# Kernel tuning notes

Measured on AMD Instinct MI355X. Metric: run time of the kernel, lower is better.

The kernel has to match this reference:

```python
import jax, jax.numpy as jnp
import numpy as np

CONF_THRES = 0.8
NMS_THRES = 0.4
IMG_SIZE = 416
MAX_DET = 3000
NEG = jnp.float32(-1e9)


def xywh2xyxy(b):
    cx, cy, w, h = b[..., 0], b[..., 1], b[..., 2], b[..., 3]
    return jnp.stack([cx - w / 2, cy - h / 2, cx + w / 2, cy + h / 2], axis=-1)


def iou_one_vs_all(box, boxes):
    # box [4], boxes [N,4]; matches original bbox_iou (+1 pixel convention, 1e-16 eps)
    ix1 = jnp.maximum(box[0], boxes[:, 0])
    iy1 = jnp.maximum(box[1], boxes[:, 1])
    ix2 = jnp.minimum(box[2], boxes[:, 2])
    iy2 = jnp.minimum(box[3], boxes[:, 3])
    inter = jnp.clip(ix2 - ix1 + 1, 0) * jnp.clip(iy2 - iy1 + 1, 0)
    a1 = (box[2] - box[0] + 1) * (box[3] - box[1] + 1)
    a2 = (boxes[:, 2] - boxes[:, 0] + 1) * (boxes[:, 3] - boxes[:, 1] + 1)
    return inter / (a1 + a2 - inter + 1e-16)


def nms_single(pred):
    # pred [N, 85] = [cx, cy, w, h, obj, 80 class scores]
    boxes = xywh2xyxy(pred[:, :4])
    obj = pred[:, 4]
    cls_conf = jnp.max(pred[:, 5:], axis=1)
    cls_id = jnp.argmax(pred[:, 5:], axis=1).astype(pred.dtype)
    valid = obj >= CONF_THRES
    score = jnp.where(valid, obj * cls_conf, NEG)
    order = jnp.argsort(-score)  # descending score, invalid pushed to end
    boxes, obj = boxes[order], obj[order]
    cls_conf, cls_id = cls_conf[order], cls_id[order]
    alive0 = valid[order]

    def step(alive, _):
        any_alive = jnp.any(alive)
        idx = jnp.argmax(alive)  # first surviving = highest remaining score
        iou = iou_one_vs_all(boxes[idx], boxes)
        invalid = (iou > NMS_THRES) & (cls_id == cls_id[idx]) & alive
        w = jnp.where(invalid, obj, 0.0)
        wsum = jnp.where(any_alive, w.sum(), 1.0)
        merged = (w[:, None] * boxes).sum(0) / wsum  # obj-weighted box merge, as original
        det = jnp.concatenate([merged, jnp.stack([obj[idx], cls_conf[idx], cls_id[idx]])])
        det = jnp.where(any_alive, det, NEG)
        return alive & ~invalid, (det, any_alive)

    _, (kept, kept_mask) = jax.lax.scan(step, alive0, None, length=MAX_DET)
    return kept, kept_mask  # kept [MAX_DET,7] = [x1,y1,x2,y2,obj,cls_conf,cls_id]


def setup_inputs() -> dict:
    key = jax.random.key(0)
    k1, k2, k3, k4 = jax.random.split(key, 4)
    B, N, C = 16, 10647, 80
    cxy = jax.random.uniform(k1, (B, N, 2), jnp.float32) * IMG_SIZE   # box centers in pixels
    wh = jax.random.uniform(k2, (B, N, 2), jnp.float32) * 80.0 + 2.0  # box sizes
    obj = jax.random.uniform(k3, (B, N, 1), jnp.float32)              # objectness
    cls = jax.random.uniform(k4, (B, N, C), jnp.float32)              # class scores
    return {"detections": jnp.concatenate([cxy, wh, obj, cls], axis=-1)}


def reference(detections):
    # NMS on every image (original non_max_suppression iterates whole batch)
    kept, kept_mask = jax.vmap(nms_single)(detections)
    # YoloModel.forward: take image 0, columns [class_conf, class_id],
    # sort ascending by class_conf then flip -> descending; return probs.
    conf0 = jnp.where(kept_mask[0], kept[0, :, 5], NEG)
    probs = -jnp.sort(-conf0)  # padded slots are NEG at the tail
    return probs
```

## Files before the change

kernel.cpp:

```cpp
#include <hip/hip_runtime.h>

#pragma clang fp contract(off)

#define N_BOX   10647
#define N_CLS   80
#define ROW     85
#define CONF_T  0.8f
#define NMS_T   0.4f
#define NEGV    -1000000000.0f
#define KMAX    256
#define OUT_N   3000
#define SURV_N  4096
#define NBLK    80
#define NTHR    256
#define ROWS_PB 136
#define CTR_STRIDE 32
#define CTR_SURV (80 * CTR_STRIDE)
#define CTR_BAR  (81 * CTR_STRIDE)
#define CTR_BYTES (82 * 128)

typedef unsigned long long u64;
typedef unsigned int u32;

#define AT_LD64(p)   __hip_atomic_load((p),  __ATOMIC_RELAXED, __HIP_MEMORY_SCOPE_AGENT)
#define AT_ST64(p,v) __hip_atomic_store((p), (v), __ATOMIC_RELAXED, __HIP_MEMORY_SCOPE_AGENT)
#define AT_LD32(p)   __hip_atomic_load((p),  __ATOMIC_RELAXED, __HIP_MEMORY_SCOPE_AGENT)
#define AT_ST32(p,v) __hip_atomic_store((p), (v), __ATOMIC_RELAXED, __HIP_MEMORY_SCOPE_AGENT)
#define AT_LDF(p)    __hip_atomic_load((p),  __ATOMIC_RELAXED, __HIP_MEMORY_SCOPE_AGENT)
#define AT_STF(p,v)  __hip_atomic_store((p), (v), __ATOMIC_RELAXED, __HIP_MEMORY_SCOPE_AGENT)

__device__ __forceinline__ u64 pack_ff(float a, float b) {
    union { float f[2]; u64 u; } x; x.f[0] = a; x.f[1] = b; return x.u;
}
__device__ __forceinline__ u64 pack_fi(float a, int b) {
    union { struct { float f; int i; } s; u64 u; } x; x.s.f = a; x.s.i = b; return x.u;
}
__device__ __forceinline__ float lo_f(u64 v) { union { u64 u; float f[2]; } x; x.u = v; return x.f[0]; }
__device__ __forceinline__ float hi_f(u64 v) { union { u64 u; float f[2]; } x; x.u = v; return x.f[1]; }
__device__ __forceinline__ int   hi_i(u64 v) { union { u64 u; int i[2]; } x; x.u = v; return x.i[1]; }

__device__ __forceinline__ void grid_bar(int* bar, int target) {
    __syncthreads();
    if (threadIdx.x == 0) {
        __builtin_amdgcn_s_waitcnt(0);
        __hip_atomic_fetch_add(bar, 1, __ATOMIC_RELAXED, __HIP_MEMORY_SCOPE_AGENT);
        long guard = 0;
        while (__hip_atomic_load(bar, __ATOMIC_RELAXED, __HIP_MEMORY_SCOPE_AGENT) < target) {
            __builtin_amdgcn_s_sleep(2);
            if (++guard > (1L << 26)) break;
        }
    }
    __syncthreads();
}

__global__ __launch_bounds__(NTHR) void k_fused(const float* __restrict__ det,
                                                float* __restrict__ out,
                                                int* counters,
                                                u64* pA, u64* pB, u64* pS, u32* pC,
                                                float* surv) {
    __shared__ float lds[ROWS_PB * ROW];
    __shared__ int nkeep, base;
    const int tid  = threadIdx.x;
    const int bid  = blockIdx.x;
    const int gidx = bid * NTHR + tid;
    int* bar = counters + CTR_BAR;

    {
        const int row0 = bid * ROWS_PB;
        int nrows = N_BOX - row0;
        if (nrows > ROWS_PB) nrows = ROWS_PB;
        if (nrows > 0) {
            const int nflt = nrows * ROW;
            const float* src = det + (size_t)row0 * ROW;
            const int n4 = nflt >> 2;
            float4* l4 = (float4*)lds;
            const float4* s4 = (const float4*)src;
            #pragma unroll 4
            for (int j = tid; j < n4; j += NTHR) l4[j] = s4[j];
            for (int j = (n4 << 2) + tid; j < nflt; j += NTHR) lds[j] = src[j];
            __syncthreads();
            if (tid < nrows) {
                const float* p = lds + tid * ROW;
                float obj = p[4];
                if (obj >= CONF_T) {
                    float cx = p[0], cy = p[1], w = p[2], h = p[3];
                    float hw = w / 2.0f, hh = h / 2.0f;
                    float best = p[5]; int bcls = 0;
                    for (int c = 1; c < N_CLS; ++c) {
                        float v = p[5 + c];
                        if (v > best) { best = v; bcls = c; }
                    }
                    int pos = atomicAdd(&counters[bcls * CTR_STRIDE], 1);
                    if (pos < KMAX) {
                        int o = bcls * KMAX + pos;
                        AT_ST64(&pA[o], pack_ff(cx - hw, cy - hh));
                        AT_ST64(&pB[o], pack_ff(cx + hw, cy + hh));
                        AT_ST64(&pS[o], pack_fi(obj * best, row0 + tid));
                        AT_ST32(&pC[o], __float_as_uint(best));
                    }
                }
            }
        }
    }
    grid_bar(bar, NBLK);

    {
        float* rsc   = lds;
        int*   ridx  = (int*)(lds + KMAX);
        float* sx1   = lds + 2 * KMAX;
        float* sy1   = lds + 3 * KMAX;
        float* sx2   = lds + 4 * KMAX;
        float* sy2   = lds + 5 * KMAX;
        float* scf   = lds + 6 * KMAX;
        float* keepc = lds + 7 * KMAX;
        unsigned char* alive = (unsigned char*)(lds + 8 * KMAX);

        const int c = bid;
        if (tid == 0) nkeep = 0;
        int k = AT_LD32((u32*)&counters[c * CTR_STRIDE]);
        if (k > KMAX) k = KMAX;

        for (int i = tid; i < k; i += NTHR) {
            u64 si = AT_LD64(&pS[c * KMAX + i]);
            rsc[i] = lo_f(si); ridx[i] = hi_i(si);
        }
        __syncthreads();

        for (int i = tid; i < k; i += NTHR) {
            float s = rsc[i]; int id = ridx[i]; int r = 0;
            for (int j = 0; j < k; ++j) {
                float sj = rsc[j];
                r += (sj > s) || (sj == s && ridx[j] < id);
            }
            int o = c * KMAX + i;
            u64 a = AT_LD64(&pA[o]);
            u64 b = AT_LD64(&pB[o]);
            sx1[r] = lo_f(a); sy1[r] = hi_f(a);
            sx2[r] = lo_f(b); sy2[r] = hi_f(b);
            scf[r] = __uint_as_float(AT_LD32(&pC[o]));
            alive[r] = 1;
        }
        __syncthreads();

        for (int i = 0; i < k; ++i) {
            bool a = (alive[i] != 0);
            __syncthreads();
            if (a) {
                if (tid == 0) { keepc[nkeep++] = scf[i]; alive[i] = 0; }
                float px1 = sx1[i], py1 = sy1[i], px2 = sx2[i], py2 = sy2[i];
                float a1 = ((px2 - px1) + 1.0f) * ((py2 - py1) + 1.0f);
                for (int j = i + 1 + tid; j < k; j += NTHR) {
                    if (!alive[j]) continue;
                    float ix1 = fmaxf(px1, sx1[j]);
                    float iy1 = fmaxf(py1, sy1[j]);
                    float ix2 = fminf(px2, sx2[j]);
                    float iy2 = fminf(py2, sy2[j]);
                    float iw = fmaxf((ix2 - ix1) + 1.0f, 0.0f);
                    float ih = fmaxf((iy2 - iy1) + 1.0f, 0.0f);
                    float inter = iw * ih;
                    float a2 = ((sx2[j] - sx1[j]) + 1.0f) * ((sy2[j] - sy1[j]) + 1.0f);
                    float den = ((a1 + a2) - inter) + 1e-16f;
                    if (inter / den > NMS_T) alive[j] = 0;
                }
            }
            __syncthreads();
        }

        if (tid == 0) base = atomicAdd(&counters[CTR_SURV], nkeep);
        __syncthreads();
        int nb = nkeep, b = base;
        for (int i = tid; i < nb; i += NTHR) {
            int o = b + i;
            if (o < SURV_N) AT_STF(&surv[o], keepc[i]);
        }
    }
    grid_bar(bar, 2 * NBLK);

    {
        int m = AT_LD32((u32*)&counters[CTR_SURV]); if (m > SURV_N) m = SURV_N;
        float* slds = lds;
        for (int i = tid; i < m; i += NTHR) slds[i] = AT_LDF(&surv[i]);
        __syncthreads();

        const int lane = tid & 63;
        const int wid  = gidx >> 6;
        for (int g = wid; g < m; g += NBLK * (NTHR / 64)) {
            const float v = slds[g];
            int cnt = 0;
            for (int j = lane; j < m; j += 64) {
                float sj = slds[j];
                cnt += (sj > v) || (sj == v && j < g);
            }
            #pragma unroll
            for (int off = 32; off > 0; off >>= 1) cnt += __shfl_down(cnt, off, 64);
            if (lane == 0 && cnt < OUT_N) out[cnt] = v;
        }
        for (int i = m + gidx; i < OUT_N; i += NBLK * NTHR) out[i] = NEGV;
    }
}

extern "C" void kernel_launch(void* const* d_in, const int* in_sizes, int n_in,
                              void* d_out, int out_size, void* d_ws, size_t ws_size,
                              hipStream_t stream) {
    const float* det = (const float*)d_in[0];
    float* out = (float*)d_out;

    const size_t NB = (size_t)N_CLS * KMAX;
    char* p = (char*)d_ws;
    int*   counters = (int*)p;  p += 16384;
    u64*   pA   = (u64*)p;      p += NB * 8;
    u64*   pB   = (u64*)p;      p += NB * 8;
    u64*   pS   = (u64*)p;      p += NB * 8;
    u32*   pC   = (u32*)p;      p += NB * 4;
    float* surv = (float*)p;

    hipMemsetAsync(d_ws, 0, CTR_BYTES, stream);
    hipLaunchKernelGGL(k_fused, dim3(NBLK), dim3(NTHR), 0, stream,
                       det, out, counters, pA, pB, pS, pC, surv);
}
```

Before: 48.30 us.

## Split fused persistent kernel into three launches replacing grid barriers

Replaces the single 80-block persistent kernel and its spin-wait grid barriers with three separate kernels: filter/stage, per-class NMS, and final rank. The staging kernel now uses many more, smaller blocks (56 rows each), so the input read spreads across more CUs. Output padding with NEG is moved into the staging kernel, and the relaxed atomic loads and stores become plain accesses because kernel boundaries now provide the ordering. The cost is two extra kernel launch gaps in exchange for removing the atomic barrier spins and the low-parallelism load phase.

```diff
diff --git a/kernel.cpp b/kernel.cpp
--- a/kernel.cpp
+++ b/kernel.cpp
@@ -11,23 +11,14 @@
 #define KMAX    256
 #define OUT_N   3000
 #define SURV_N  4096
-#define NBLK    80
-#define NTHR    256
-#define ROWS_PB 136
+#define ROWS_PB 56
+#define NBLK_B  ((N_BOX + ROWS_PB - 1) / ROWS_PB)
 #define CTR_STRIDE 32
 #define CTR_SURV (80 * CTR_STRIDE)
-#define CTR_BAR  (81 * CTR_STRIDE)
 #define CTR_BYTES (82 * 128)
 
 typedef unsigned long long u64;
 typedef unsigned int u32;
-
-#define AT_LD64(p)   __hip_atomic_load((p),  __ATOMIC_RELAXED, __HIP_MEMORY_SCOPE_AGENT)
-#define AT_ST64(p,v) __hip_atomic_store((p), (v), __ATOMIC_RELAXED, __HIP_MEMORY_SCOPE_AGENT)
-#define AT_LD32(p)   __hip_atomic_load((p),  __ATOMIC_RELAXED, __HIP_MEMORY_SCOPE_AGENT)
-#define AT_ST32(p,v) __hip_atomic_store((p), (v), __ATOMIC_RELAXED, __HIP_MEMORY_SCOPE_AGENT)
-#define AT_LDF(p)    __hip_atomic_load((p),  __ATOMIC_RELAXED, __HIP_MEMORY_SCOPE_AGENT)
-#define AT_STF(p,v)  __hip_atomic_store((p), (v), __ATOMIC_RELAXED, __HIP_MEMORY_SCOPE_AGENT)
 
 __device__ __forceinline__ u64 pack_ff(float a, float b) {
     union { float f[2]; u64 u; } x; x.f[0] = a; x.f[1] = b; return x.u;
@@ -39,163 +30,150 @@
 __device__ __forceinline__ float hi_f(u64 v) { union { u64 u; float f[2]; } x; x.u = v; return x.f[1]; }
 __device__ __forceinline__ int   hi_i(u64 v) { union { u64 u; int i[2]; } x; x.u = v; return x.i[1]; }
 
-__device__ __forceinline__ void grid_bar(int* bar, int target) {
-    __syncthreads();
-    if (threadIdx.x == 0) {
-        __builtin_amdgcn_s_waitcnt(0);
-        __hip_atomic_fetch_add(bar, 1, __ATOMIC_RELAXED, __HIP_MEMORY_SCOPE_AGENT);
-        long guard = 0;
-        while (__hip_atomic_load(bar, __ATOMIC_RELAXED, __HIP_MEMORY_SCOPE_AGENT) < target) {
-            __builtin_amdgcn_s_sleep(2);
-            if (++guard > (1L << 26)) break;
-        }
-    }
-    __syncthreads();
-}
-
-__global__ __launch_bounds__(NTHR) void k_fused(const float* __restrict__ det,
-                                                float* __restrict__ out,
-                                                int* counters,
-                                                u64* pA, u64* pB, u64* pS, u32* pC,
-                                                float* surv) {
+__global__ __launch_bounds__(256) void k_stage(const float* __restrict__ det,
+                                               float* __restrict__ out,
+                                               int* __restrict__ counters,
+                                               u64* __restrict__ pA,
+                                               u64* __restrict__ pB,
+                                               u64* __restrict__ pS,
+                                               u32* __restrict__ pC) {
     __shared__ float lds[ROWS_PB * ROW];
-    __shared__ int nkeep, base;
     const int tid  = threadIdx.x;
     const int bid  = blockIdx.x;
-    const int gidx = bid * NTHR + tid;
-    int* bar = counters + CTR_BAR;
-
-    {
-        const int row0 = bid * ROWS_PB;
-        int nrows = N_BOX - row0;
-        if (nrows > ROWS_PB) nrows = ROWS_PB;
-        if (nrows > 0) {
-            const int nflt = nrows * ROW;
-            const float* src = det + (size_t)row0 * ROW;
-            const int n4 = nflt >> 2;
-            float4* l4 = (float4*)lds;
-            const float4* s4 = (const float4*)src;
-            #pragma unroll 4
-            for (int j = tid; j < n4; j += NTHR) l4[j] = s4[j];
-            for (int j = (n4 << 2) + tid; j < nflt; j += NTHR) lds[j] = src[j];
-            __syncthreads();
-            if (tid < nrows) {
-                const float* p = lds + tid * ROW;
-                float obj = p[4];
-                if (obj >= CONF_T) {
-                    float cx = p[0], cy = p[1], w = p[2], h = p[3];
-                    float hw = w / 2.0f, hh = h / 2.0f;
-                    float best = p[5]; int bcls = 0;
-                    for (int c = 1; c < N_CLS; ++c) {
-                        float v = p[5 + c];
-                        if (v > best) { best = v; bcls = c; }
-                    }
-                    int pos = atomicAdd(&counters[bcls * CTR_STRIDE], 1);
-                    if (pos < KMAX) {
-                        int o = bcls * KMAX + pos;
-                        AT_ST64(&pA[o], pack_ff(cx - hw, cy - hh));
-                        AT_ST64(&pB[o], pack_ff(cx + hw, cy + hh));
-                        AT_ST64(&pS[o], pack_fi(obj * best, row0 + tid));
-                        AT_ST32(&pC[o], __float_as_uint(best));
-                    }
-                }
+    const int gidx = bid * 256 + tid;
+
+    if (gidx < OUT_N) out[gidx] = NEGV;
+
+    const int row0 = bid * ROWS_PB;
+    int nrows = N_BOX - row0; if (nrows > ROWS_PB) nrows = ROWS_PB;
+    if (nrows <= 0) return;
+
+    const int nflt = nrows * ROW;
+    const float* src = det + (size_t)row0 * ROW;
+    const int n4 = nflt >> 2;
+    float4* l4 = (float4*)lds;
+    const float4* s4 = (const float4*)src;
+    for (int j = tid; j < n4; j += 256) l4[j] = s4[j];
+    for (int j = (n4 << 2) + tid; j < nflt; j += 256) lds[j] = src[j];
+    __syncthreads();
+
+    if (tid < nrows) {
+        const float* p = lds + tid * ROW;
+        float obj = p[4];
+        if (obj >= CONF_T) {
+            float cx = p[0], cy = p[1], w = p[2], h = p[3];
+            float hw = w / 2.0f, hh = h / 2.0f;
+            float best = p[5]; int bcls = 0;
+            for (int c = 1; c < N_CLS; ++c) {
+                float v = p[5 + c];
+                if (v > best) { best = v; bcls = c; }
             }
-        }
-    }
-    grid_bar(bar, NBLK);
-
-    {
-        float* rsc   = lds;
-        int*   ridx  = (int*)(lds + KMAX);
-        float* sx1   = lds + 2 * KMAX;
-        float* sy1   = lds + 3 * KMAX;
-        float* sx2   = lds + 4 * KMAX;
-        float* sy2   = lds + 5 * KMAX;
-        float* scf   = lds + 6 * KMAX;
-        float* keepc = lds + 7 * KMAX;
-        unsigned char* alive = (unsigned char*)(lds + 8 * KMAX);
-
-        const int c = bid;
-        if (tid == 0) nkeep = 0;
-        int k = AT_LD32((u32*)&counters[c * CTR_STRIDE]);
-        if (k > KMAX) k = KMAX;
-
-        for (int i = tid; i < k; i += NTHR) {
-            u64 si = AT_LD64(&pS[c * KMAX + i]);
-            rsc[i] = lo_f(si); ridx[i] = hi_i(si);
-        }
+            int pos = atomicAdd(&counters[bcls * CTR_STRIDE], 1);
+            if (pos < KMAX) {
+                int o = bcls * KMAX + pos;
+                pA[o] = pack_ff(cx - hw, cy - hh);
+                pB[o] = pack_ff(cx + hw, cy + hh);
+                pS[o] = pack_fi(obj * best, row0 + tid);
+                pC[o] = __float_as_uint(best);
+            }
+        }
+    }
+}
+
+__global__ __launch_bounds__(256) void k_nms(const u64* __restrict__ pA,
+                                             const u64* __restrict__ pB,
+                                             const u64* __restrict__ pS,
+                                             const u32* __restrict__ pC,
+                                             int* __restrict__ counters,
+                                             float* __restrict__ surv) {
+    __shared__ float rsc[KMAX]; __shared__ int ridx[KMAX];
+    __shared__ float sx1[KMAX], sy1[KMAX], sx2[KMAX], sy2[KMAX], scf[KMAX];
+    __shared__ unsigned char alive[KMAX];
+    __shared__ float keepc[KMAX];
+    __shared__ int nkeep, base;
+
+    const int c = blockIdx.x;
+    const int tid = threadIdx.x;
+    if (tid == 0) nkeep = 0;
+
+    int k = counters[c * CTR_STRIDE]; if (k > KMAX) k = KMAX;
+
+    for (int i = tid; i < k; i += 256) {
+        u64 si = pS[c * KMAX + i];
+        rsc[i] = lo_f(si); ridx[i] = hi_i(si);
+    }
+    __syncthreads();
+
+    for (int i = tid; i < k; i += 256) {
+        float s = rsc[i]; int id = ridx[i]; int r = 0;
+        for (int j = 0; j < k; ++j) {
+            float sj = rsc[j];
+            r += (sj > s) || (sj == s && ridx[j] < id);
+        }
+        int o = c * KMAX + i;
+        u64 a = pA[o], b = pB[o];
+        sx1[r] = lo_f(a); sy1[r] = hi_f(a);
+        sx2[r] = lo_f(b); sy2[r] = hi_f(b);
+        scf[r] = __uint_as_float(pC[o]);
+        alive[r] = 1;
+    }
+    __syncthreads();
+
+    for (int i = 0; i < k; ++i) {
+        bool a = (alive[i] != 0);
         __syncthreads();
-
-        for (int i = tid; i < k; i += NTHR) {
-            float s = rsc[i]; int id = ridx[i]; int r = 0;
-            for (int j = 0; j < k; ++j) {
-                float sj = rsc[j];
-                r += (sj > s) || (sj == s && ridx[j] < id);
+        if (a) {
+            if (tid == 0) { keepc[nkeep++] = scf[i]; alive[i] = 0; }
+            float px1 = sx1[i], py1 = sy1[i], px2 = sx2[i], py2 = sy2[i];
+            float a1 = ((px2 - px1) + 1.0f) * ((py2 - py1) + 1.0f);
+            for (int j = i + 1 + tid; j < k; j += 256) {
+                if (!alive[j]) continue;
+                float ix1 = fmaxf(px1, sx1[j]);
+                float iy1 = fmaxf(py1, sy1[j]);
+                float ix2 = fminf(px2, sx2[j]);
+                float iy2 = fminf(py2, sy2[j]);
+                float iw = fmaxf((ix2 - ix1) + 1.0f, 0.0f);
+                float ih = fmaxf((iy2 - iy1) + 1.0f, 0.0f);
+                float inter = iw * ih;
+                float a2 = ((sx2[j] - sx1[j]) + 1.0f) * ((sy2[j] - sy1[j]) + 1.0f);
+                float den = ((a1 + a2) - inter) + 1e-16f;
+                if (inter / den > NMS_T) alive[j] = 0;
             }
-            int o = c * KMAX + i;
-            u64 a = AT_LD64(&pA[o]);
-            u64 b = AT_LD64(&pB[o]);
-            sx1[r] = lo_f(a); sy1[r] = hi_f(a);
-            sx2[r] = lo_f(b); sy2[r] = hi_f(b);
-            scf[r] = __uint_as_float(AT_LD32(&pC[o]));
-            alive[r] = 1;
         }
         __syncthreads();
-
-        for (int i = 0; i < k; ++i) {
-            bool a = (alive[i] != 0);
-            __syncthreads();
-            if (a) {
-                if (tid == 0) { keepc[nkeep++] = scf[i]; alive[i] = 0; }
-                float px1 = sx1[i], py1 = sy1[i], px2 = sx2[i], py2 = sy2[i];
-                float a1 = ((px2 - px1) + 1.0f) * ((py2 - py1) + 1.0f);
-                for (int j = i + 1 + tid; j < k; j += NTHR) {
-                    if (!alive[j]) continue;
-                    float ix1 = fmaxf(px1, sx1[j]);
-                    float iy1 = fmaxf(py1, sy1[j]);
-                    float ix2 = fminf(px2, sx2[j]);
-                    float iy2 = fminf(py2, sy2[j]);
-                    float iw = fmaxf((ix2 - ix1) + 1.0f, 0.0f);
-                    float ih = fmaxf((iy2 - iy1) + 1.0f, 0.0f);
-                    float inter = iw * ih;
-                    float a2 = ((sx2[j] - sx1[j]) + 1.0f) * ((sy2[j] - sy1[j]) + 1.0f);
-                    float den = ((a1 + a2) - inter) + 1e-16f;
-                    if (inter / den > NMS_T) alive[j] = 0;
-                }
-            }
-            __syncthreads();
-        }
-
-        if (tid == 0) base = atomicAdd(&counters[CTR_SURV], nkeep);
-        __syncthreads();
-        int nb = nkeep, b = base;
-        for (int i = tid; i < nb; i += NTHR) {
-            int o = b + i;
-            if (o < SURV_N) AT_STF(&surv[o], keepc[i]);
-        }
-    }
-    grid_bar(bar, 2 * NBLK);
-
-    {
-        int m = AT_LD32((u32*)&counters[CTR_SURV]); if (m > SURV_N) m = SURV_N;
-        float* slds = lds;
-        for (int i = tid; i < m; i += NTHR) slds[i] = AT_LDF(&surv[i]);
-        __syncthreads();
-
-        const int lane = tid & 63;
-        const int wid  = gidx >> 6;
-        for (int g = wid; g < m; g += NBLK * (NTHR / 64)) {
-            const float v = slds[g];
-            int cnt = 0;
-            for (int j = lane; j < m; j += 64) {
-                float sj = slds[j];
-                cnt += (sj > v) || (sj == v && j < g);
-            }
-            #pragma unroll
-            for (int off = 32; off > 0; off >>= 1) cnt += __shfl_down(cnt, off, 64);
-            if (lane == 0 && cnt < OUT_N) out[cnt] = v;
-        }
-        for (int i = m + gidx; i < OUT_N; i += NBLK * NTHR) out[i] = NEGV;
+    }
+
+    if (tid == 0) base = atomicAdd(&counters[CTR_SURV], nkeep);
+    __syncthreads();
+    int nb = nkeep, b = base;
+    for (int i = tid; i < nb; i += 256) {
+        int o = b + i;
+        if (o < SURV_N) surv[o] = keepc[i];
+    }
+}
+
+__global__ __launch_bounds__(256) void k_rank(const float* __restrict__ surv,
+                                              const int* __restrict__ counters,
+                                              float* __restrict__ out) {
+    __shared__ float slds[SURV_N];
+    const int tid = threadIdx.x;
+    int m = counters[CTR_SURV]; if (m > SURV_N) m = SURV_N;
+
+    for (int i = tid; i < m; i += 256) slds[i] = surv[i];
+    __syncthreads();
+
+    const int lane = tid & 63;
+    const int wid  = (blockIdx.x * 256 + tid) >> 6;
+    for (int g = wid; g < m; g += N_CLS * 4) {
+        const float v = slds[g];
+        int cnt = 0;
+        for (int j = lane; j < m; j += 64) {
+            float sj = slds[j];
+            cnt += (sj > v) || (sj == v && j < g);
+        }
+        #pragma unroll
+        for (int off = 32; off > 0; off >>= 1) cnt += __shfl_down(cnt, off, 64);
+        if (lane == 0 && cnt < OUT_N) out[cnt] = v;
     }
 }
 
@@ -214,7 +192,11 @@
     u32*   pC   = (u32*)p;      p += NB * 4;
     float* surv = (float*)p;
 
-    hipMemsetAsync(d_ws, 0, CTR_BYTES, stream);
-    hipLaunchKernelGGL(k_fused, dim3(NBLK), dim3(NTHR), 0, stream,
-                       det, out, counters, pA, pB, pS, pC, surv);
-}
+    hipMemsetAsync(counters, 0, CTR_BYTES, stream);
+    hipLaunchKernelGGL(k_stage, dim3(NBLK_B), dim3(256), 0, stream,
+                       det, out, counters, pA, pB, pS, pC);
+    hipLaunchKernelGGL(k_nms,   dim3(N_CLS), dim3(256), 0, stream,
+                       pA, pB, pS, pC, counters, surv);
+    hipLaunchKernelGGL(k_rank,  dim3(N_CLS), dim3(256), 0, stream,
+                       surv, counters, out);
+}
```

Measured after the change: 45.48 us. 1.06x faster.
